# Optimization experiments

Measured on AMD Instinct MI355X. Metric: run time of the kernel, lower is better.

## Reference

```python
import jax, jax.numpy as jnp
import numpy as np

B, P, G, E = 2, 16, 128, 96
C110, C011, C001 = 4, 2, 1
N, CO = 128, 2

def _pw(x, W, b):
    """1x1 conv of any spatial rank == pointwise channel mixing."""
    y = jnp.einsum('oc,bc...->bo...', W, x)
    return y + b.reshape((1, -1) + (1,) * (y.ndim - 2))

def _hidden(s110, s011, s001, Ws, bs):
    # s110:[B,C,P,G,1]  s011:[B,C,1,G,E]  s001:[B,C,1,1,E]
    # sub-stream order: [110 full, 110 pool-P, 110 pool-G, 011 full, 011 pool-G, 011 pool-E, 001]
    t110 = s110[..., 0]         # [B,C,P,G]
    t011 = s011[:, :, 0]        # [B,C,G,E]
    t001 = s001[:, :, 0, 0]     # [B,C,E]
    s = (_pw(t110, Ws[0], bs[0])[..., None]
         + _pw(t110.max(axis=2), Ws[1], bs[1])[:, :, None, :, None]
         + _pw(t110.max(axis=3), Ws[2], bs[2])[:, :, :, None, None]
         + _pw(t011, Ws[3], bs[3])[:, :, None, :, :]
         + _pw(t011.max(axis=2), Ws[4], bs[4])[:, :, None, None, :]
         + _pw(t011.max(axis=3), Ws[5], bs[5])[:, :, None, :, None]
         + _pw(t001, Ws[6], bs[6])[:, :, None, None, :])
    s = jax.nn.leaky_relu(s)    # [B,N,P,G,E]
    return (jnp.max(s, axis=4, keepdims=True),
            jnp.max(s, axis=2, keepdims=True),
            jnp.max(s, axis=(2, 3), keepdims=True))

def _forward(x110, x011, x001, W0_110, b0_110, W0_011, b0_011, W0_001, b0_001, W1, b1, Wact, bact, Wcrit, bcrit):
    Ws0 = [W0_110[0], W0_110[1], W0_110[2], W0_011[0], W0_011[1], W0_011[2], W0_001]
    bs0 = [b0_110[0], b0_110[1], b0_110[2], b0_011[0], b0_011[1], b0_011[2], b0_001]
    s110, s011, s001 = _hidden(x110, x011, x001, Ws0, bs0)
    s110, s011, s001 = _hidden(s110, s011, s001, list(W1), list(b1))
    t110 = s110[..., 0]  # [B,N,P,G]
    # actor head: eliminate G,E via mean pooling (dim_elimination_max_pooling=False)
    a110 = _pw(t110.mean(axis=3), Wact[0], bact[0])              # [B,CO,P]
    a011 = _pw(s011.mean(axis=(3, 4)), Wact[1], bact[1])         # [B,CO,1]
    a001 = _pw(s001[:, :, :, 0].mean(axis=3), Wact[2], bact[2])  # [B,CO,1]
    actions = jax.nn.leaky_relu(a110 + a011 + a001)              # [B,CO,P]
    # critic head: eliminate G via mean pooling
    c110 = _pw(t110.mean(axis=3), Wcrit[0], bcrit[0])            # [B,CO,P]
    c011 = _pw(s011[:, :, 0].mean(axis=2), Wcrit[1], bcrit[1])   # [B,CO,E]
    c001 = _pw(s001[:, :, 0, 0], Wcrit[2], bcrit[2])             # [B,CO,E]
    v = jax.nn.leaky_relu(c110[:, :, :, None] + (c011 + c001)[:, :, None, :])  # [B,CO,P,E]
    v110 = v.max(axis=3).sum(axis=2)  # stream (1,1,0): max over E, sum over P
    v011 = v.max(axis=2).sum(axis=2)  # streams (0,1,1) and (0,0,1) coincide numerically
    values = (2.0 + v110 + 2.0 * v011).reshape(-1)  # python sum(l, 2) starts at 2
    return actions, values

def setup_inputs() -> dict:
    key = jax.random.key(0)
    ks = jax.random.split(key, 12)
    f32 = jnp.float32
    def w(k, shape, fan):
        return jax.random.normal(k, shape, f32) / np.float32(np.sqrt(fan))
    return {
        'x110': jax.random.normal(ks[0], (B, C110, P, G, 1), f32),
        'x011': jax.random.normal(ks[1], (B, C011, 1, G, E), f32),
        'x001': jax.random.normal(ks[2], (B, C001, 1, 1, E), f32),
        'W0_110': w(ks[3], (3, N, C110), C110), 'b0_110': jnp.zeros((3, N), f32),
        'W0_011': w(ks[4], (3, N, C011), C011), 'b0_011': jnp.zeros((3, N), f32),
        'W0_001': w(ks[5], (N, C001), C001),    'b0_001': jnp.zeros((N,), f32),
        'W1':     w(ks[6], (7, N, N), N),       'b1':     jnp.zeros((7, N), f32),
        'Wact':   w(ks[7], (3, CO, N), N),      'bact':   jnp.zeros((3, CO), f32),
        'Wcrit':  w(ks[8], (3, CO, N), N),      'bcrit':  jnp.zeros((3, CO), f32),
    }

def reference(x110, x011, x001, W0_110, b0_110, W0_011, b0_011, W0_001, b0_001, W1, b1, Wact, bact, Wcrit, bcrit):
    return _forward(x110, x011, x001, W0_110, b0_110, W0_011, b0_011, W0_001, b0_001, W1, b1, Wact, bact, Wcrit, bcrit)
```

## Files before the change

kernel.cpp:

```cpp
#include <hip/hip_runtime.h>
#include <math.h>

#define DEVI __device__ __forceinline__

constexpr int B = 2, P = 16, G = 128, E = 96, N = 128, CO = 2;

DEVI float lrelu(float x) { return x > 0.f ? x : 0.01f * x; }

constexpr int OFF_U1     = 0;
constexpr int OFF_V1     = OFF_U1 + 524288;
constexpr int OFF_MAXPU0 = OFF_V1 + 3145728;
constexpr int OFF_MAXEV0 = OFF_MAXPU0 + 32768;
constexpr int OFF_MP110  = OFF_MAXEV0 + 32768;
constexpr int OFF_MG110  = OFF_MP110 + 32768;
constexpr int OFF_S001A  = OFF_MG110 + 4096;
constexpr int OFF_RMP    = OFF_S001A + 24576;
constexpr int OFF_RMG    = OFF_RMP + 1024;
constexpr int OFF_RME    = OFF_RMG + 128;
constexpr int OFF_RMG011 = OFF_RME + 512;
constexpr int OFF_WT     = OFF_RMG011 + 384;
constexpr int OFF_PART   = OFF_WT + 81920;

__global__ void __launch_bounds__(256) k_layer0(
    const float* __restrict__ x110, const float* __restrict__ x011,
    const float* __restrict__ x001,
    const float* __restrict__ W0_110, const float* __restrict__ b0_110,
    const float* __restrict__ W0_011, const float* __restrict__ b0_011,
    const float* __restrict__ W0_001, const float* __restrict__ b0_001,
    const float* __restrict__ W1,
    float* __restrict__ maxpU0g, float* __restrict__ maxeV0g,
    float* __restrict__ mp110, float* __restrict__ mg110,
    float* __restrict__ s001a,
    float* __restrict__ rmpG, float* __restrict__ rmgG,
    float* __restrict__ rmeG, float* __restrict__ rmg011G,
    float* __restrict__ wT) {
  __shared__ float xs[4 * 16 * 128];
  __shared__ float v0h[64 * 97];
  __shared__ float u0[16 * 128];
  __shared__ float rmp[512], rmgS[64], rme[256], rmg011L[192];
  __shared__ float mpu[128], mev[128], part[256];
  const int bn = blockIdx.x, b = bn >> 7, n = bn & 127, tid = threadIdx.x;

  {
    const float4* xsrc = (const float4*)(x110 + (size_t)b * 8192);
    float4* xdst = (float4*)xs;
#pragma unroll
    for (int k = 0; k < 8; k++) xdst[tid + k * 256] = xsrc[tid + k * 256];
  }
  {
    int c = tid >> 7, g = tid & 127;
    const float4* r = (const float4*)(x011 + ((size_t)(b * 2 + c) * 128 + g) * 96);
    float m = -INFINITY;
#pragma unroll
    for (int j = 0; j < 24; j++) {
      float4 v = r[j];
      m = fmaxf(m, fmaxf(fmaxf(v.x, v.y), fmaxf(v.z, v.w)));
    }
    rme[tid] = m;
  }
  __syncthreads();
  for (int i = tid; i < 512; i += 256) {
    int c = i >> 7, g = i & 127;
    float m = -INFINITY;
    for (int p = 0; p < P; p++) m = fmaxf(m, xs[(c * 16 + p) * 128 + g]);
    rmp[i] = m;
  }
  if (tid < 64) {
    int c = tid >> 4, p = tid & 15;
    float m = -INFINITY;
    for (int g = 0; g < G; g++) m = fmaxf(m, xs[(c * 16 + p) * 128 + g]);
    rmgS[tid] = m;
  }
  if (tid < 192) {
    int c = tid / 96, e = tid % 96;
    const float* pp = x011 + ((size_t)(b * 2 + c) * 128) * 96 + e;
    float m = -INFINITY;
    for (int g = 0; g < G; g++) m = fmaxf(m, pp[g * 96]);
    rmg011L[tid] = m;
  }
  __syncthreads();
  float w0[4], w1[4], w2[4];
#pragma unroll
  for (int cc = 0; cc < 4; cc++) {
    w0[cc] = W0_110[n * 4 + cc];
    w1[cc] = W0_110[512 + n * 4 + cc];
    w2[cc] = W0_110[1024 + n * 4 + cc];
  }
  float we0 = W0_011[512 + n * 2], we1 = W0_011[512 + n * 2 + 1];
  float bu = b0_110[n] + b0_110[128 + n] + b0_110[256 + n] + b0_011[256 + n];
  float vw00 = W0_011[n * 2], vw01 = W0_011[n * 2 + 1];
  float vw10 = W0_011[256 + n * 2], vw11 = W0_011[256 + n * 2 + 1];
  float w001 = W0_001[n];
  float bv = b0_011[n] + b0_011[128 + n] + b0_001[n];

#pragma unroll
  for (int k = 0; k < 8; k++) {
    int i = tid + k * 256, p = i >> 7, g = i & 127;
    float acc = bu + we0 * rme[g] + we1 * rme[128 + g];
#pragma unroll
    for (int cc = 0; cc < 4; cc++)
      acc += w0[cc] * xs[(cc * 16 + p) * 128 + g] + w1[cc] * rmp[cc * 128 + g]
           + w2[cc] * rmgS[cc * 16 + p];
    u0[i] = acc;
  }
  __syncthreads();
  if (tid < 128) {
    float m = -INFINITY;
    for (int p = 0; p < P; p++) m = fmaxf(m, u0[p * 128 + tid]);
    mpu[tid] = m;
    maxpU0g[bn * 128 + tid] = m;
  }
  __syncthreads();

  const float* xa = x011 + (size_t)(b * 2) * 12288;
  const float* xb = xa + 12288;
  const float* xc = x001 + b * 96;
  float runMax = -INFINITY;

  for (int h2 = 0; h2 < 2; h2++) {
    for (int k = 0; k < 24; k++) {
      int i = tid + k * 256;
      int gp = i / 96, e = i - gp * 96;
      int g = h2 * 64 + gp;
      float val = bv + vw00 * xa[g * 96 + e] + vw01 * xb[g * 96 + e]
                + vw10 * rmg011L[e] + vw11 * rmg011L[96 + e] + w001 * xc[e];
      v0h[gp * 97 + e] = val;
    }
    __syncthreads();
    {
      int gp = tid & 63, q = tid >> 6;
      const float* r = &v0h[gp * 97 + q * 24];
      float m = -INFINITY;
      for (int j = 0; j < 24; j++) m = fmaxf(m, r[j]);
      part[q * 64 + gp] = m;
    }
    __syncthreads();
    if (tid < 64) {
      float m = fmaxf(fmaxf(part[tid], part[64 + tid]),
                      fmaxf(part[128 + tid], part[192 + tid]));
      int g = h2 * 64 + tid;
      mev[g] = m;
      maxeV0g[bn * 128 + g] = m;
      mp110[bn * 128 + g] = lrelu(mpu[g] + m);
    }
    if (tid < 96) {
      for (int gp = 0; gp < 64; gp++)
        runMax = fmaxf(runMax, mpu[h2 * 64 + gp] + v0h[gp * 97 + tid]);
    }
    __syncthreads();
  }
  {
    int p = tid >> 4, ch = tid & 15;
    float m = -INFINITY;
    for (int g = ch * 8; g < ch * 8 + 8; g++)
      m = fmaxf(m, u0[p * 128 + g] + mev[g]);
    part[tid] = m;
  }
  if (tid < 96) s001a[bn * 96 + tid] = lrelu(runMax);
  __syncthreads();
  if (tid < 16) {
    float m = -INFINITY;
    for (int ch = 0; ch < 16; ch++) m = fmaxf(m, part[tid * 16 + ch]);
    mg110[bn * 16 + tid] = lrelu(m);
  }
  if (n == 0) {
    for (int i = tid; i < 512; i += 256) rmpG[b * 512 + i] = rmp[i];
    if (tid < 64) rmgG[b * 64 + tid] = rmgS[tid];
    rmeG[b * 256 + tid] = rme[tid];
    if (tid < 192) rmg011G[b * 192 + tid] = rmg011L[tid];
  }
  {
    const int gt = bn * 256 + tid;
#pragma unroll
    for (int it = 0; it < 2; it++) {
      int idx = gt + it * 65536;
      if (idx < 81920) {
        int m = idx >> 14, r = idx & 16383;
        int c = r >> 7, nn = r & 127;
        float v;
        if (m == 0)      v = W1[nn * 128 + c];
        else if (m == 1) v = W1[16384 + nn * 128 + c] + W1[5 * 16384 + nn * 128 + c];
        else if (m == 2) v = W1[2 * 16384 + nn * 128 + c];
        else if (m == 3) v = W1[3 * 16384 + nn * 128 + c];
        else             v = W1[4 * 16384 + nn * 128 + c] + W1[6 * 16384 + nn * 128 + c];
        wT[idx] = v;
      }
    }
  }
}

__global__ void __launch_bounds__(512) k_layer1c(
    const float* __restrict__ x110, const float* __restrict__ x011,
    const float* __restrict__ x001,
    const float* __restrict__ W0_110, const float* __restrict__ b0_110,
    const float* __restrict__ W0_011, const float* __restrict__ b0_011,
    const float* __restrict__ W0_001, const float* __restrict__ b0_001,
    const float* __restrict__ maxpU0g, const float* __restrict__ maxeV0g,
    const float* __restrict__ rmpG, const float* __restrict__ rmgG,
    const float* __restrict__ rmeG, const float* __restrict__ rmg011G,
    const float* __restrict__ wT,
    float* __restrict__ U1, float* __restrict__ V1) {
  __shared__ float s110c[128 * 16];
  __shared__ float s011c[128 * 96];
  __shared__ float W0L110[1536], W0L011[768], W0L001[128];
  __shared__ float busum[128], bvsum[128], mpu[128], mev[128];
  __shared__ float x011row[192], rmg011s[192], x001s[96];
  __shared__ float x110col[64], rmg110p[64], rmp4[4], rme2[2];
  const int blk = blockIdx.x;
  const int b = blk >> 7, g = blk & 127;
  const int tid = threadIdx.x;

  for (int i = tid; i < 1536; i += 512) W0L110[i] = W0_110[i];
  for (int i = tid; i < 768; i += 512) W0L011[i] = W0_011[i];
  if (tid < 128) {
    W0L001[tid] = W0_001[tid];
    busum[tid] = b0_110[tid] + b0_110[128 + tid] + b0_110[256 + tid]
               + b0_011[256 + tid];
    bvsum[tid] = b0_011[tid] + b0_011[128 + tid] + b0_001[tid];
    mpu[tid] = maxpU0g[(b * 128 + tid) * 128 + g];
    mev[tid] = maxeV0g[(b * 128 + tid) * 128 + g];
  } else if (tid >= 256 && tid < 448) {
    int i = tid - 256;
    int c = i / 96, e = i % 96;
    x011row[i] = x011[((size_t)(b * 2 + c) * 128 + g) * 96 + e];
    rmg011s[i] = rmg011G[b * 192 + i];
  } else if (tid >= 448 && tid < 512) {
    int i = tid - 448;
    int c = i >> 4, p = i & 15;
    x110col[i] = x110[((size_t)(b * 4 + c) * 16 + p) * 128 + g];
    rmg110p[i] = rmgG[b * 64 + i];
  } else if (tid >= 128 && tid < 224) {
    x001s[tid - 128] = x001[b * 96 + tid - 128];
  } else if (tid >= 224 && tid < 228) {
    rmp4[tid - 224] = rmpG[(b * 4 + tid - 224) * 128 + g];
  } else if (tid >= 228 && tid < 230) {
    rme2[tid - 228] = rmeG[(b * 2 + tid - 228) * 128 + g];
  }
  __syncthreads();

#pragma unroll
  for (int k = 0; k < 4; k++) {
    int i = tid + k * 512, c = i >> 4, p = i & 15;
    float acc = busum[c] + W0L011[512 + c * 2] * rme2[0]
              + W0L011[512 + c * 2 + 1] * rme2[1];
#pragma unroll
    for (int cc = 0; cc < 4; cc++)
      acc += W0L110[c * 4 + cc] * x110col[cc * 16 + p]
           + W0L110[512 + c * 4 + cc] * rmp4[cc]
           + W0L110[1024 + c * 4 + cc] * rmg110p[cc * 16 + p];
    s110c[i] = lrelu(acc + mev[c]);
  }
  for (int k = 0; k < 24; k++) {
    int i = tid + k * 512;
    int c = i / 96, e = i - c * 96;
    float v = bvsum[c]
            + W0L011[c * 2] * x011row[e] + W0L011[c * 2 + 1] * x011row[96 + e]
            + W0L011[256 + c * 2] * rmg011s[e]
            + W0L011[256 + c * 2 + 1] * rmg011s[96 + e]
            + W0L001[c] * x001s[e];
    s011c[i] = lrelu(v + mpu[c]);
  }
  __syncthreads();

  const float* w0T = wT;
  const float* w3T = wT + 3 * 16384;

  if (tid < 256) {
    int n0 = (tid >> 3) * 4, e0 = (tid & 7) * 12;
    float4 acc[4][3];
#pragma unroll
    for (int ni = 0; ni < 4; ni++)
#pragma unroll
      for (int k = 0; k < 3; k++) acc[ni][k] = make_float4(0.f, 0.f, 0.f, 0.f);
    for (int c = 0; c < 128; c++) {
      float4 wv = *(const float4*)&w3T[c * 128 + n0];
      float4 s0 = *(const float4*)&s011c[c * 96 + e0];
      float4 s1 = *(const float4*)&s011c[c * 96 + e0 + 4];
      float4 s2 = *(const float4*)&s011c[c * 96 + e0 + 8];
#pragma unroll
      for (int ni = 0; ni < 4; ni++) {
        float wc = ni == 0 ? wv.x : ni == 1 ? wv.y : ni == 2 ? wv.z : wv.w;
        acc[ni][0].x += wc * s0.x; acc[ni][0].y += wc * s0.y;
        acc[ni][0].z += wc * s0.z; acc[ni][0].w += wc * s0.w;
        acc[ni][1].x += wc * s1.x; acc[ni][1].y += wc * s1.y;
        acc[ni][1].z += wc * s1.z; acc[ni][1].w += wc * s1.w;
        acc[ni][2].x += wc * s2.x; acc[ni][2].y += wc * s2.y;
        acc[ni][2].z += wc * s2.z; acc[ni][2].w += wc * s2.w;
      }
    }
#pragma unroll
    for (int ni = 0; ni < 4; ni++) {
      float* dst = V1 + ((size_t)((b * 128 + g) * 128 + n0 + ni)) * 96 + e0;
#pragma unroll
      for (int k = 0; k < 3; k++) *(float4*)(dst + k * 4) = acc[ni][k];
    }
  } else {
    int t = tid - 256;
    int n = t & 127, ph = t >> 7;
    float a[8];
#pragma unroll
    for (int j = 0; j < 8; j++) a[j] = 0.f;
    for (int c = 0; c < 128; c++) {
      float w0v = w0T[c * 128 + n];
      float4 s0 = *(const float4*)&s110c[c * 16 + ph * 8];
      float4 s1 = *(const float4*)&s110c[c * 16 + ph * 8 + 4];
      a[0] += w0v * s0.x; a[1] += w0v * s0.y; a[2] += w0v * s0.z; a[3] += w0v * s0.w;
      a[4] += w0v * s1.x; a[5] += w0v * s1.y; a[6] += w0v * s1.z; a[7] += w0v * s1.w;
    }
    float* dst = U1 + ((size_t)((b * 128 + g) * 16 + ph * 8)) * 128 + n;
#pragma unroll
    for (int j = 0; j < 8; j++) dst[j * 128] = a[j];
  }
}

__global__ void __launch_bounds__(256) k_post3(
    const float* __restrict__ U1, const float* __restrict__ V1,
    const float* __restrict__ s001a, const float* __restrict__ mp110,
    const float* __restrict__ mg110,
    const float* __restrict__ wT, const float* __restrict__ b1,
    float* __restrict__ partOut) {
  constexpr int GS = 16;
  __shared__ float Vt[GS][8][104];
  __shared__ float Ut[GS][16][9];
  __shared__ float bfL[8][GS];
  __shared__ float egL[8][96];
  __shared__ float cpL[8][16];
  __shared__ float partE[GS][8][4];
  __shared__ float mxeV[GS][8], mxpU[GS][8];
  __shared__ float bbL[8], bvL[8];
  const int blk = blockIdx.x;
  const int b = blk >> 7, nc = (blk >> 3) & 15, gc = blk & 7;
  const int n0 = nc * 8, g0 = gc * 16;
  const int tid = threadIdx.x;
  const float* w15T = wT + 16384;
  const float* w2T  = wT + 2 * 16384;
  const float* w46T = wT + 4 * 16384;

  if (tid < 8) {
    int n = n0 + tid;
    bbL[tid] = b1[n] + b1[128 + n] + b1[256 + n] + b1[640 + n];
    bvL[tid] = b1[384 + n] + b1[512 + n] + b1[768 + n];
  }
  if (tid < 128) {
    int nn = tid >> 4, gl = tid & 15;
    float acc = 0.f;
    for (int c = 0; c < 128; c++)
      acc += w15T[c * 128 + n0 + nn] * mp110[(b * 128 + c) * 128 + g0 + gl];
    bfL[nn][gl] = acc;
  } else {
    int i = tid - 128;
    int nn = i >> 4, p = i & 15;
    float acc = 0.f;
    for (int c = 0; c < 128; c++)
      acc += w2T[c * 128 + n0 + nn] * mg110[(b * 128 + c) * 16 + p];
    cpL[nn][p] = acc;
  }
#pragma unroll
  for (int k = 0; k < 3; k++) {
    int s = tid + k * 256;
    int nn = s / 96, e = s % 96;
    float acc = 0.f;
    for (int c = 0; c < 128; c++)
      acc += w46T[c * 128 + n0 + nn] * s001a[b * 12288 + c * 96 + e];
    egL[nn][e] = acc;
  }
  __syncthreads();

  const size_t Ubase = (size_t)b * 128 * 16 * 128;
  const size_t Vbase = (size_t)b * 128 * 128 * 96;
#pragma unroll
  for (int k = 0; k < 12; k++) {
    int i4 = tid + k * 256;
    int gs = i4 / 192, r = i4 % 192, nn = r / 24, e4 = r % 24;
    float4 v = *(const float4*)(V1 + Vbase
                 + ((size_t)(g0 + gs) * 128 + n0 + nn) * 96 + e4 * 4);
    float bvv = bvL[nn];
    const float* eg = &egL[nn][e4 * 4];
    float4 o = make_float4(v.x + bvv + eg[0], v.y + bvv + eg[1],
                           v.z + bvv + eg[2], v.w + bvv + eg[3]);
    *(float4*)&Vt[gs][nn][e4 * 4] = o;
  }
#pragma unroll
  for (int k = 0; k < 8; k++) {
    int i = tid + k * 256;
    int gs = i >> 7, r = i & 127, p = r >> 3, nn = r & 7;
    float u = U1[Ubase + ((size_t)(g0 + gs) * 16 + p) * 128 + n0 + nn];
    Ut[gs][p][nn] = u + bbL[nn] + cpL[nn][p] + bfL[nn][gs];
  }
  __syncthreads();
#pragma unroll
  for (int k = 0; k < 2; k++) {
    int i = tid + k * 256;
    int gs = i >> 5, nn = (i >> 2) & 7, ec = i & 3;
    float m = -INFINITY;
    for (int e = ec * 24; e < ec * 24 + 24; e++) m = fmaxf(m, Vt[gs][nn][e]);
    partE[gs][nn][ec] = m;
  }
  __syncthreads();
  if (tid < 128) {
    int gs = tid >> 3, nn = tid & 7;
    mxeV[gs][nn] = fmaxf(fmaxf(partE[gs][nn][0], partE[gs][nn][1]),
                         fmaxf(partE[gs][nn][2], partE[gs][nn][3]));
    float m = -INFINITY;
    for (int p = 0; p < 16; p++) m = fmaxf(m, Ut[gs][p][nn]);
    mxpU[gs][nn] = m;
  }
  __syncthreads();

  float* pb = partOut + (size_t)blk * 1664;
  if (tid < 128) {
    int nn = tid >> 4, p = tid & 15;
    float a = 0.f;
#pragma unroll
    for (int gs = 0; gs < GS; gs++)
      a += lrelu(Ut[gs][p][nn] + mxeV[gs][nn]);
    pb[tid] = a;
  }
#pragma unroll
  for (int k = 0; k < 3; k++) {
    int s = tid + k * 256;
    int nn = s / 96, e = s % 96;
    float a = 0.f, m = -INFINITY;
#pragma unroll
    for (int gs = 0; gs < GS; gs++) {
      float pre = mxpU[gs][nn] + Vt[gs][nn][e];
      a += lrelu(pre);
      m = fmaxf(m, pre);
    }
    pb[128 + s] = a;
    pb[896 + s] = m;
  }
}

__global__ void __launch_bounds__(256) k_final(
    const float* __restrict__ partIn,
    const float* __restrict__ Wact, const float* __restrict__ bact,
    const float* __restrict__ Wcrit, const float* __restrict__ bcrit,
    float* __restrict__ out) {
  __shared__ float buf[128][97];
  __shared__ float m110s[128][17];
  __shared__ float sm011[N], sm001[N], sce1[E], sce[E], scp[P], srow[P], scol[E];
  const int bo = blockIdx.x;
  const int o = bo & 1, b = bo >> 1;
  const int t = threadIdx.x;
  const float* pbB = partIn + (size_t)(b * 16) * 8 * 1664;

#pragma unroll
  for (int k = 0; k < 8; k++) {
    int i = t + k * 256;
    int nc = i >> 7, j = i & 127;
    const float* base = pbB + (size_t)(nc * 8) * 1664;
    float a = 0.f;
#pragma unroll
    for (int gc = 0; gc < 8; gc++) a += base[gc * 1664 + j];
    m110s[nc * 8 + (j >> 4)][j & 15] = a * (1.f / G);
  }
#pragma unroll
  for (int k = 0; k < 48; k++) {
    int i = t + k * 256;
    int nc = i / 768, r = i % 768;
    const float* base = pbB + (size_t)(nc * 8) * 1664;
    float a = 0.f;
#pragma unroll
    for (int gc = 0; gc < 8; gc++) a += base[gc * 1664 + 128 + r];
    buf[nc * 8 + r / 96][r % 96] = a * (1.f / G);
  }
  __syncthreads();
  if (t < 128) {
    float s = 0.f;
    for (int e = 0; e < E; e++) s += buf[t][e];
    sm011[t] = s * (1.f / E);
  }
  if (t < 96) {
    const float* wc1 = Wcrit + (1 * CO + o) * N;
    float c = 0.f;
    for (int n = 0; n < N; n++) c += wc1[n] * buf[n][t];
    sce1[t] = c;
  }
  __syncthreads();
#pragma unroll
  for (int k = 0; k < 48; k++) {
    int i = t + k * 256;
    int nc = i / 768, r = i % 768;
    const float* base = pbB + (size_t)(nc * 8) * 1664;
    float m = -INFINITY;
#pragma unroll
    for (int gc = 0; gc < 8; gc++) m = fmaxf(m, base[gc * 1664 + 896 + r]);
    buf[nc * 8 + r / 96][r % 96] = lrelu(m);
  }
  __syncthreads();
  if (t < 128) {
    float s = 0.f;
    for (int e = 0; e < E; e++) s += buf[t][e];
    sm001[t] = s * (1.f / E);
  }
  if (t < 96) {
    const float* wc2 = Wcrit + (2 * CO + o) * N;
    float c = 0.f;
    for (int n = 0; n < N; n++) c += wc2[n] * buf[n][t];
    sce[t] = sce1[t] + c + bcrit[CO + o] + bcrit[2 * CO + o];
  }
  __syncthreads();
  if (t < P) {
    const float* wa0 = Wact + o * N;
    const float* wa1 = Wact + (1 * CO + o) * N;
    const float* wa2 = Wact + (2 * CO + o) * N;
    const float* wc0 = Wcrit + o * N;
    float a = 0.f, c = 0.f, aa = 0.f;
    for (int n = 0; n < N; n++) {
      float m = m110s[n][t];
      a += wa0[n] * m;
      c += wc0[n] * m;
      aa += wa1[n] * sm011[n] + wa2[n] * sm001[n];
    }
    float act = a + aa + bact[o] + bact[CO + o] + bact[2 * CO + o];
    out[(b * CO + o) * P + t] = lrelu(act);
    scp[t] = c + bcrit[o];
  }
  __syncthreads();
  if (t < P) {
    float m = -INFINITY;
    for (int e = 0; e < E; e++) m = fmaxf(m, lrelu(scp[t] + sce[e]));
    srow[t] = m;
  } else if (t < P + E) {
    int e = t - P;
    float m = -INFINITY;
    for (int p = 0; p < P; p++) m = fmaxf(m, lrelu(scp[p] + sce[e]));
    scol[e] = m;
  }
  __syncthreads();
  if (t == 0) {
    float v110 = 0.f, v011 = 0.f;
    for (int p = 0; p < P; p++) v110 += srow[p];
    for (int e = 0; e < E; e++) v011 += scol[e];
    out[B * CO * P + b * CO + o] = 2.f + v110 + 2.f * v011;
  }
}

extern "C" void kernel_launch(void* const* d_in, const int* in_sizes, int n_in,
                              void* d_out, int out_size, void* d_ws, size_t ws_size,
                              hipStream_t stream) {
  const float* x110   = (const float*)d_in[0];
  const float* x011   = (const float*)d_in[1];
  const float* x001   = (const float*)d_in[2];
  const float* W0_110 = (const float*)d_in[3];
  const float* b0_110 = (const float*)d_in[4];
  const float* W0_011 = (const float*)d_in[5];
  const float* b0_011 = (const float*)d_in[6];
  const float* W0_001 = (const float*)d_in[7];
  const float* b0_001 = (const float*)d_in[8];
  const float* W1     = (const float*)d_in[9];
  const float* b1     = (const float*)d_in[10];
  const float* Wact   = (const float*)d_in[11];
  const float* bact   = (const float*)d_in[12];
  const float* Wcrit  = (const float*)d_in[13];
  const float* bcrit  = (const float*)d_in[14];
  float* out = (float*)d_out;
  float* w = (float*)d_ws;

  float* U1     = w + OFF_U1;
  float* V1     = w + OFF_V1;
  float* maxpU0 = w + OFF_MAXPU0;
  float* maxeV0 = w + OFF_MAXEV0;
  float* mp110  = w + OFF_MP110;
  float* mg110  = w + OFF_MG110;
  float* s001a  = w + OFF_S001A;
  float* rmpG   = w + OFF_RMP;
  float* rmgG   = w + OFF_RMG;
  float* rmeG   = w + OFF_RME;
  float* rmg011 = w + OFF_RMG011;
  float* wT     = w + OFF_WT;
  float* partB  = w + OFF_PART;

  k_layer0<<<256, 256, 0, stream>>>(x110, x011, x001, W0_110, b0_110, W0_011,
                                    b0_011, W0_001, b0_001, W1,
                                    maxpU0, maxeV0, mp110, mg110, s001a,
                                    rmpG, rmgG, rmeG, rmg011, wT);
  k_layer1c<<<256, 512, 0, stream>>>(x110, x011, x001, W0_110, b0_110, W0_011,
                                     b0_011, W0_001, b0_001,
                                     maxpU0, maxeV0, rmpG, rmgG, rmeG, rmg011,
                                     wT, U1, V1);
  k_post3<<<256, 256, 0, stream>>>(U1, V1, s001a, mp110, mg110, wT, b1, partB);
  k_final<<<4, 256, 0, stream>>>(partB, Wact, bact, Wcrit, bcrit, out);
}
```

Baseline: 119.9 us.

## Split layer kernels across G/N halves and move input reductions to a prep kernel

Measured after the change: 133.3 us. 1.11x slower.

```diff
diff --git a/kernel.cpp b/kernel.cpp
--- a/kernel.cpp
+++ b/kernel.cpp
@@ -9,17 +9,67 @@
 
 constexpr int OFF_U1     = 0;
 constexpr int OFF_V1     = OFF_U1 + 524288;
-constexpr int OFF_MAXPU0 = OFF_V1 + 3145728;
-constexpr int OFF_MAXEV0 = OFF_MAXPU0 + 32768;
-constexpr int OFF_MP110  = OFF_MAXEV0 + 32768;
-constexpr int OFF_MG110  = OFF_MP110 + 32768;
-constexpr int OFF_S001A  = OFF_MG110 + 4096;
-constexpr int OFF_RMP    = OFF_S001A + 24576;
+constexpr int OFF_MP110  = OFF_V1 + 3145728;
+constexpr int OFF_MGP    = OFF_MP110 + 32768;
+constexpr int OFF_S1P    = OFF_MGP + 8192;
+constexpr int OFF_RMP    = OFF_S1P + 49152;
 constexpr int OFF_RMG    = OFF_RMP + 1024;
 constexpr int OFF_RME    = OFF_RMG + 128;
 constexpr int OFF_RMG011 = OFF_RME + 512;
 constexpr int OFF_WT     = OFF_RMG011 + 384;
 constexpr int OFF_PART   = OFF_WT + 81920;
+
+__global__ void __launch_bounds__(256) k_prep(
+    const float* __restrict__ x110, const float* __restrict__ x011,
+    const float* __restrict__ W1,
+    float* __restrict__ rmpG, float* __restrict__ rmgG,
+    float* __restrict__ rmeG, float* __restrict__ rmg011G,
+    float* __restrict__ wT) {
+  const int blk = blockIdx.x, tid = threadIdx.x;
+  if (blk < 56) {
+    for (int idx = blk * 256 + tid; idx < 81920; idx += 56 * 256) {
+      int m = idx >> 14, r = idx & 16383;
+      int c = r >> 7, nn = r & 127;
+      float v;
+      if (m == 0)      v = W1[nn * 128 + c];
+      else if (m == 1) v = W1[16384 + nn * 128 + c] + W1[5 * 16384 + nn * 128 + c];
+      else if (m == 2) v = W1[2 * 16384 + nn * 128 + c];
+      else if (m == 3) v = W1[3 * 16384 + nn * 128 + c];
+      else             v = W1[4 * 16384 + nn * 128 + c] + W1[6 * 16384 + nn * 128 + c];
+      wT[idx] = v;
+    }
+  } else {
+    int t = (blk - 56) * 256 + tid;
+    if (t < 1024) {
+      int g = t & 127, c = (t >> 7) & 3, b = t >> 9;
+      const float* base = x110 + ((b * 4 + c) * P) * G + g;
+      float m = -INFINITY;
+      for (int p = 0; p < P; p++) m = fmaxf(m, base[p * G]);
+      rmpG[t] = m;
+    } else if (t < 1152) {
+      int i = t - 1024;
+      int p = i & 15, c = (i >> 4) & 3, b = i >> 6;
+      const float* base = x110 + ((b * 4 + c) * P + p) * G;
+      float m = -INFINITY;
+      for (int g = 0; g < G; g++) m = fmaxf(m, base[g]);
+      rmgG[i] = m;
+    } else if (t < 1664) {
+      int i = t - 1152;
+      int g = i & 127, c = (i >> 7) & 1, b = i >> 8;
+      const float* base = x011 + ((size_t)(b * 2 + c) * G + g) * E;
+      float m = -INFINITY;
+      for (int e = 0; e < E; e++) m = fmaxf(m, base[e]);
+      rmeG[i] = m;
+    } else if (t < 2048) {
+      int i = t - 1664;
+      int e = i % 96; int r = i / 96; int c = r & 1, b = r >> 1;
+      const float* base = x011 + ((size_t)(b * 2 + c) * G) * E + e;
+      float m = -INFINITY;
+      for (int g = 0; g < G; g++) m = fmaxf(m, base[g * E]);
+      rmg011G[i] = m;
+    }
+  }
+}
 
 __global__ void __launch_bounds__(256) k_layer0(
     const float* __restrict__ x110, const float* __restrict__ x011,
@@ -27,58 +77,40 @@
     const float* __restrict__ W0_110, const float* __restrict__ b0_110,
     const float* __restrict__ W0_011, const float* __restrict__ b0_011,
     const float* __restrict__ W0_001, const float* __restrict__ b0_001,
-    const float* __restrict__ W1,
-    float* __restrict__ maxpU0g, float* __restrict__ maxeV0g,
-    float* __restrict__ mp110, float* __restrict__ mg110,
-    float* __restrict__ s001a,
-    float* __restrict__ rmpG, float* __restrict__ rmgG,
-    float* __restrict__ rmeG, float* __restrict__ rmg011G,
-    float* __restrict__ wT) {
-  __shared__ float xs[4 * 16 * 128];
+    const float* __restrict__ rmpG, const float* __restrict__ rmgG,
+    const float* __restrict__ rmeG, const float* __restrict__ rmg011G,
+    float* __restrict__ mp110, float* __restrict__ mgp,
+    float* __restrict__ s1p) {
+  __shared__ float xs[4 * 16 * 64];
   __shared__ float v0h[64 * 97];
-  __shared__ float u0[16 * 128];
-  __shared__ float rmp[512], rmgS[64], rme[256], rmg011L[192];
-  __shared__ float mpu[128], mev[128], part[256];
-  const int bn = blockIdx.x, b = bn >> 7, n = bn & 127, tid = threadIdx.x;
-
-  {
-    const float4* xsrc = (const float4*)(x110 + (size_t)b * 8192);
-    float4* xdst = (float4*)xs;
-#pragma unroll
-    for (int k = 0; k < 8; k++) xdst[tid + k * 256] = xsrc[tid + k * 256];
-  }
-  {
-    int c = tid >> 7, g = tid & 127;
-    const float4* r = (const float4*)(x011 + ((size_t)(b * 2 + c) * 128 + g) * 96);
-    float m = -INFINITY;
-#pragma unroll
-    for (int j = 0; j < 24; j++) {
-      float4 v = r[j];
-      m = fmaxf(m, fmaxf(fmaxf(v.x, v.y), fmaxf(v.z, v.w)));
-    }
-    rme[tid] = m;
-  }
-  __syncthreads();
-  for (int i = tid; i < 512; i += 256) {
-    int c = i >> 7, g = i & 127;
-    float m = -INFINITY;
-    for (int p = 0; p < P; p++) m = fmaxf(m, xs[(c * 16 + p) * 128 + g]);
-    rmp[i] = m;
-  }
-  if (tid < 64) {
-    int c = tid >> 4, p = tid & 15;
-    float m = -INFINITY;
-    for (int g = 0; g < G; g++) m = fmaxf(m, xs[(c * 16 + p) * 128 + g]);
-    rmgS[tid] = m;
-  }
-  if (tid < 192) {
-    int c = tid / 96, e = tid % 96;
-    const float* pp = x011 + ((size_t)(b * 2 + c) * 128) * 96 + e;
-    float m = -INFINITY;
-    for (int g = 0; g < G; g++) m = fmaxf(m, pp[g * 96]);
-    rmg011L[tid] = m;
-  }
-  __syncthreads();
+  __shared__ float u0h[16 * 64];
+  __shared__ float rmpL[256], rmeL[128], rmgSL[64], rmg011L[192], x001L[96];
+  __shared__ float mpu[64], mev[64], part[256];
+  const int blk = blockIdx.x;
+  const int b = blk >> 8, n = (blk >> 1) & 127, gh = blk & 1;
+  const int bn = b * 128 + n, g0 = gh * 64;
+  const int tid = threadIdx.x;
+
+#pragma unroll
+  for (int k = 0; k < 4; k++) {
+    int i4 = tid + k * 256;
+    int g4 = i4 & 15, p = (i4 >> 4) & 15, cc = i4 >> 8;
+    *(float4*)&xs[(cc * 16 + p) * 64 + g4 * 4] =
+        *(const float4*)(x110 + ((size_t)(b * 4 + cc) * 16 + p) * 128 + g0 + g4 * 4);
+  }
+  if (tid < 256) {
+    int cc = tid >> 6, gp = tid & 63;
+    rmpL[tid] = rmpG[b * 512 + cc * 128 + g0 + gp];
+  }
+  if (tid < 128) {
+    int c2 = tid >> 6, gp = tid & 63;
+    rmeL[tid] = rmeG[b * 256 + c2 * 128 + g0 + gp];
+  }
+  if (tid < 64) rmgSL[tid] = rmgG[b * 64 + tid];
+  if (tid < 192) rmg011L[tid] = rmg011G[b * 192 + tid];
+  if (tid < 96) x001L[tid] = x001[b * 96 + tid];
+  __syncthreads();
+
   float w0[4], w1[4], w2[4];
 #pragma unroll
   for (int cc = 0; cc < 4; cc++) {
@@ -94,108 +126,76 @@
   float bv = b0_011[n] + b0_011[128 + n] + b0_001[n];
 
 #pragma unroll
-  for (int k = 0; k < 8; k++) {
-    int i = tid + k * 256, p = i >> 7, g = i & 127;
-    float acc = bu + we0 * rme[g] + we1 * rme[128 + g];
+  for (int k = 0; k < 4; k++) {
+    int i = tid + k * 256, p = i >> 6, gp = i & 63;
+    float acc = bu + we0 * rmeL[gp] + we1 * rmeL[64 + gp];
 #pragma unroll
     for (int cc = 0; cc < 4; cc++)
-      acc += w0[cc] * xs[(cc * 16 + p) * 128 + g] + w1[cc] * rmp[cc * 128 + g]
-           + w2[cc] * rmgS[cc * 16 + p];
-    u0[i] = acc;
-  }
-  __syncthreads();
-  if (tid < 128) {
-    float m = -INFINITY;
-    for (int p = 0; p < P; p++) m = fmaxf(m, u0[p * 128 + tid]);
-    mpu[tid] = m;
-    maxpU0g[bn * 128 + tid] = m;
-  }
-  __syncthreads();
-
-  const float* xa = x011 + (size_t)(b * 2) * 12288;
-  const float* xb = xa + 12288;
-  const float* xc = x001 + b * 96;
-  float runMax = -INFINITY;
-
-  for (int h2 = 0; h2 < 2; h2++) {
+      acc += w0[cc] * xs[(cc * 16 + p) * 64 + gp] + w1[cc] * rmpL[cc * 64 + gp]
+           + w2[cc] * rmgSL[cc * 16 + p];
+    u0h[i] = acc;
+  }
+  {
+    const float* xa = x011 + (size_t)(b * 2) * 12288;
+    const float* xb = xa + 12288;
+#pragma unroll
     for (int k = 0; k < 24; k++) {
       int i = tid + k * 256;
       int gp = i / 96, e = i - gp * 96;
-      int g = h2 * 64 + gp;
+      int g = g0 + gp;
       float val = bv + vw00 * xa[g * 96 + e] + vw01 * xb[g * 96 + e]
-                + vw10 * rmg011L[e] + vw11 * rmg011L[96 + e] + w001 * xc[e];
+                + vw10 * rmg011L[e] + vw11 * rmg011L[96 + e] + w001 * x001L[e];
       v0h[gp * 97 + e] = val;
     }
-    __syncthreads();
-    {
-      int gp = tid & 63, q = tid >> 6;
-      const float* r = &v0h[gp * 97 + q * 24];
-      float m = -INFINITY;
-      for (int j = 0; j < 24; j++) m = fmaxf(m, r[j]);
-      part[q * 64 + gp] = m;
-    }
-    __syncthreads();
-    if (tid < 64) {
-      float m = fmaxf(fmaxf(part[tid], part[64 + tid]),
-                      fmaxf(part[128 + tid], part[192 + tid]));
-      int g = h2 * 64 + tid;
-      mev[g] = m;
-      maxeV0g[bn * 128 + g] = m;
-      mp110[bn * 128 + g] = lrelu(mpu[g] + m);
-    }
-    if (tid < 96) {
-      for (int gp = 0; gp < 64; gp++)
-        runMax = fmaxf(runMax, mpu[h2 * 64 + gp] + v0h[gp * 97 + tid]);
-    }
-    __syncthreads();
-  }
+  }
+  __syncthreads();
+  {
+    int gp = tid & 63, q = tid >> 6;
+    const float* r = &v0h[gp * 97 + q * 24];
+    float m = -INFINITY;
+    for (int j = 0; j < 24; j++) m = fmaxf(m, r[j]);
+    part[q * 64 + gp] = m;
+  }
+  if (tid < 64) {
+    float m = -INFINITY;
+    for (int p = 0; p < P; p++) m = fmaxf(m, u0h[p * 64 + tid]);
+    mpu[tid] = m;
+  }
+  __syncthreads();
+  if (tid < 64) {
+    float m = fmaxf(fmaxf(part[tid], part[64 + tid]),
+                    fmaxf(part[128 + tid], part[192 + tid]));
+    mev[tid] = m;
+    mp110[bn * 128 + g0 + tid] = lrelu(mpu[tid] + m);
+  }
+  __syncthreads();
   {
     int p = tid >> 4, ch = tid & 15;
     float m = -INFINITY;
-    for (int g = ch * 8; g < ch * 8 + 8; g++)
-      m = fmaxf(m, u0[p * 128 + g] + mev[g]);
+    for (int gp = ch * 4; gp < ch * 4 + 4; gp++)
+      m = fmaxf(m, u0h[p * 64 + gp] + mev[gp]);
     part[tid] = m;
   }
-  if (tid < 96) s001a[bn * 96 + tid] = lrelu(runMax);
   __syncthreads();
   if (tid < 16) {
     float m = -INFINITY;
     for (int ch = 0; ch < 16; ch++) m = fmaxf(m, part[tid * 16 + ch]);
-    mg110[bn * 16 + tid] = lrelu(m);
-  }
-  if (n == 0) {
-    for (int i = tid; i < 512; i += 256) rmpG[b * 512 + i] = rmp[i];
-    if (tid < 64) rmgG[b * 64 + tid] = rmgS[tid];
-    rmeG[b * 256 + tid] = rme[tid];
-    if (tid < 192) rmg011G[b * 192 + tid] = rmg011L[tid];
-  }
-  {
-    const int gt = bn * 256 + tid;
-#pragma unroll
-    for (int it = 0; it < 2; it++) {
-      int idx = gt + it * 65536;
-      if (idx < 81920) {
-        int m = idx >> 14, r = idx & 16383;
-        int c = r >> 7, nn = r & 127;
-        float v;
-        if (m == 0)      v = W1[nn * 128 + c];
-        else if (m == 1) v = W1[16384 + nn * 128 + c] + W1[5 * 16384 + nn * 128 + c];
-        else if (m == 2) v = W1[2 * 16384 + nn * 128 + c];
-        else if (m == 3) v = W1[3 * 16384 + nn * 128 + c];
-        else             v = W1[4 * 16384 + nn * 128 + c] + W1[6 * 16384 + nn * 128 + c];
-        wT[idx] = v;
-      }
-    }
+    mgp[(bn * 2 + gh) * 16 + tid] = m;
+  }
+  if (tid < 96) {
+    float m = -INFINITY;
+    for (int gp = 0; gp < 64; gp++)
+      m = fmaxf(m, mpu[gp] + v0h[gp * 97 + tid]);
+    s1p[(bn * 2 + gh) * 96 + tid] = m;
   }
 }
 
-__global__ void __launch_bounds__(512) k_layer1c(
+__global__ void __launch_bounds__(256) k_layer1(
     const float* __restrict__ x110, const float* __restrict__ x011,
     const float* __restrict__ x001,
     const float* __restrict__ W0_110, const float* __restrict__ b0_110,
     const float* __restrict__ W0_011, const float* __restrict__ b0_011,
     const float* __restrict__ W0_001, const float* __restrict__ b0_001,
-    const float* __restrict__ maxpU0g, const float* __restrict__ maxeV0g,
     const float* __restrict__ rmpG, const float* __restrict__ rmgG,
     const float* __restrict__ rmeG, const float* __restrict__ rmg011G,
     const float* __restrict__ wT,
@@ -206,41 +206,38 @@
   __shared__ float busum[128], bvsum[128], mpu[128], mev[128];
   __shared__ float x011row[192], rmg011s[192], x001s[96];
   __shared__ float x110col[64], rmg110p[64], rmp4[4], rme2[2];
+  __shared__ float partM[256];
   const int blk = blockIdx.x;
-  const int b = blk >> 7, g = blk & 127;
+  const int b = blk >> 8, g = (blk >> 1) & 127, nh = blk & 1;
+  const int n0 = nh * 64;
   const int tid = threadIdx.x;
 
-  for (int i = tid; i < 1536; i += 512) W0L110[i] = W0_110[i];
-  for (int i = tid; i < 768; i += 512) W0L011[i] = W0_011[i];
+  for (int i = tid; i < 1536; i += 256) W0L110[i] = W0_110[i];
+  for (int i = tid; i < 768; i += 256) W0L011[i] = W0_011[i];
   if (tid < 128) {
     W0L001[tid] = W0_001[tid];
     busum[tid] = b0_110[tid] + b0_110[128 + tid] + b0_110[256 + tid]
                + b0_011[256 + tid];
     bvsum[tid] = b0_011[tid] + b0_011[128 + tid] + b0_001[tid];
-    mpu[tid] = maxpU0g[(b * 128 + tid) * 128 + g];
-    mev[tid] = maxeV0g[(b * 128 + tid) * 128 + g];
-  } else if (tid >= 256 && tid < 448) {
-    int i = tid - 256;
-    int c = i / 96, e = i % 96;
-    x011row[i] = x011[((size_t)(b * 2 + c) * 128 + g) * 96 + e];
-    rmg011s[i] = rmg011G[b * 192 + i];
-  } else if (tid >= 448 && tid < 512) {
-    int i = tid - 448;
-    int c = i >> 4, p = i & 15;
-    x110col[i] = x110[((size_t)(b * 4 + c) * 16 + p) * 128 + g];
-    rmg110p[i] = rmgG[b * 64 + i];
-  } else if (tid >= 128 && tid < 224) {
-    x001s[tid - 128] = x001[b * 96 + tid - 128];
-  } else if (tid >= 224 && tid < 228) {
-    rmp4[tid - 224] = rmpG[(b * 4 + tid - 224) * 128 + g];
-  } else if (tid >= 228 && tid < 230) {
-    rme2[tid - 228] = rmeG[(b * 2 + tid - 228) * 128 + g];
-  }
-  __syncthreads();
-
-#pragma unroll
-  for (int k = 0; k < 4; k++) {
-    int i = tid + k * 512, c = i >> 4, p = i & 15;
+  }
+  if (tid < 192) {
+    int c = tid / 96, e = tid % 96;
+    x011row[tid] = x011[((size_t)(b * 2 + c) * 128 + g) * 96 + e];
+    rmg011s[tid] = rmg011G[b * 192 + tid];
+  }
+  if (tid < 96) x001s[tid] = x001[b * 96 + tid];
+  if (tid < 64) {
+    int c = tid >> 4, p = tid & 15;
+    x110col[tid] = x110[((size_t)(b * 4 + c) * 16 + p) * 128 + g];
+    rmg110p[tid] = rmgG[b * 64 + tid];
+  }
+  if (tid < 4) rmp4[tid] = rmpG[(b * 4 + tid) * 128 + g];
+  if (tid < 2) rme2[tid] = rmeG[(b * 2 + tid) * 128 + g];
+  __syncthreads();
+
+#pragma unroll
+  for (int k = 0; k < 8; k++) {
+    int i = tid + k * 256, c = i >> 4, p = i & 15;
     float acc = busum[c] + W0L011[512 + c * 2] * rme2[0]
               + W0L011[512 + c * 2 + 1] * rme2[1];
 #pragma unroll
@@ -248,75 +245,101 @@
       acc += W0L110[c * 4 + cc] * x110col[cc * 16 + p]
            + W0L110[512 + c * 4 + cc] * rmp4[cc]
            + W0L110[1024 + c * 4 + cc] * rmg110p[cc * 16 + p];
-    s110c[i] = lrelu(acc + mev[c]);
-  }
-  for (int k = 0; k < 24; k++) {
-    int i = tid + k * 512;
+    s110c[i] = acc;
+  }
+  for (int k = 0; k < 48; k++) {
+    int i = tid + k * 256;
     int c = i / 96, e = i - c * 96;
     float v = bvsum[c]
             + W0L011[c * 2] * x011row[e] + W0L011[c * 2 + 1] * x011row[96 + e]
             + W0L011[256 + c * 2] * rmg011s[e]
             + W0L011[256 + c * 2 + 1] * rmg011s[96 + e]
             + W0L001[c] * x001s[e];
-    s011c[i] = lrelu(v + mpu[c]);
+    s011c[i] = v;
+  }
+  __syncthreads();
+  if (tid < 128) {
+    float m = -INFINITY;
+    for (int p = 0; p < P; p++) m = fmaxf(m, s110c[tid * 16 + p]);
+    mpu[tid] = m;
+  }
+  {
+    int c = tid >> 1, h = tid & 1;
+    const float* r = &s011c[c * 96 + h * 48];
+    float m = -INFINITY;
+    for (int j = 0; j < 48; j++) m = fmaxf(m, r[j]);
+    partM[tid] = m;
+  }
+  __syncthreads();
+  if (tid < 128) mev[tid] = fmaxf(partM[tid * 2], partM[tid * 2 + 1]);
+  __syncthreads();
+#pragma unroll
+  for (int k = 0; k < 8; k++) {
+    int i = tid + k * 256, c = i >> 4;
+    s110c[i] = lrelu(s110c[i] + mev[c]);
+  }
+  for (int k = 0; k < 48; k++) {
+    int i = tid + k * 256, c = i / 96;
+    s011c[i] = lrelu(s011c[i] + mpu[c]);
   }
   __syncthreads();
 
   const float* w0T = wT;
   const float* w3T = wT + 3 * 16384;
 
-  if (tid < 256) {
-    int n0 = (tid >> 3) * 4, e0 = (tid & 7) * 12;
-    float4 acc[4][3];
-#pragma unroll
-    for (int ni = 0; ni < 4; ni++)
-#pragma unroll
-      for (int k = 0; k < 3; k++) acc[ni][k] = make_float4(0.f, 0.f, 0.f, 0.f);
+  {
+    int np = tid >> 3, e0 = (tid & 7) * 12;
+    int na = n0 + np * 2, nb = na + 1;
+    float4 aA[3], aB[3];
+#pragma unroll
+    for (int k = 0; k < 3; k++) {
+      aA[k] = make_float4(0.f, 0.f, 0.f, 0.f);
+      aB[k] = make_float4(0.f, 0.f, 0.f, 0.f);
+    }
     for (int c = 0; c < 128; c++) {
-      float4 wv = *(const float4*)&w3T[c * 128 + n0];
+      float2 wv = *(const float2*)&w3T[c * 128 + na];
       float4 s0 = *(const float4*)&s011c[c * 96 + e0];
       float4 s1 = *(const float4*)&s011c[c * 96 + e0 + 4];
       float4 s2 = *(const float4*)&s011c[c * 96 + e0 + 8];
-#pragma unroll
-      for (int ni = 0; ni < 4; ni++) {
-        float wc = ni == 0 ? wv.x : ni == 1 ? wv.y : ni == 2 ? wv.z : wv.w;
-        acc[ni][0].x += wc * s0.x; acc[ni][0].y += wc * s0.y;
-        acc[ni][0].z += wc * s0.z; acc[ni][0].w += wc * s0.w;
-        acc[ni][1].x += wc * s1.x; acc[ni][1].y += wc * s1.y;
-        acc[ni][1].z += wc * s1.z; acc[ni][1].w += wc * s1.w;
-        acc[ni][2].x += wc * s2.x; acc[ni][2].y += wc * s2.y;
-        acc[ni][2].z += wc * s2.z; acc[ni][2].w += wc * s2.w;
-      }
-    }
-#pragma unroll
-    for (int ni = 0; ni < 4; ni++) {
-      float* dst = V1 + ((size_t)((b * 128 + g) * 128 + n0 + ni)) * 96 + e0;
-#pragma unroll
-      for (int k = 0; k < 3; k++) *(float4*)(dst + k * 4) = acc[ni][k];
-    }
-  } else {
-    int t = tid - 256;
-    int n = t & 127, ph = t >> 7;
-    float a[8];
-#pragma unroll
-    for (int j = 0; j < 8; j++) a[j] = 0.f;
+      aA[0].x += wv.x * s0.x; aA[0].y += wv.x * s0.y;
+      aA[0].z += wv.x * s0.z; aA[0].w += wv.x * s0.w;
+      aA[1].x += wv.x * s1.x; aA[1].y += wv.x * s1.y;
+      aA[1].z += wv.x * s1.z; aA[1].w += wv.x * s1.w;
+      aA[2].x += wv.x * s2.x; aA[2].y += wv.x * s2.y;
+      aA[2].z += wv.x * s2.z; aA[2].w += wv.x * s2.w;
+      aB[0].x += wv.y * s0.x; aB[0].y += wv.y * s0.y;
+      aB[0].z += wv.y * s0.z; aB[0].w += wv.y * s0.w;
+      aB[1].x += wv.y * s1.x; aB[1].y += wv.y * s1.y;
+      aB[1].z += wv.y * s1.z; aB[1].w += wv.y * s1.w;
+      aB[2].x += wv.y * s2.x; aB[2].y += wv.y * s2.y;
+      aB[2].z += wv.y * s2.z; aB[2].w += wv.y * s2.w;
+    }
+    float* dA = V1 + ((size_t)((b * 128 + g) * 128 + na)) * 96 + e0;
+    float* dB = dA + 96;
+#pragma unroll
+    for (int k = 0; k < 3; k++) {
+      *(float4*)(dA + k * 4) = aA[k];
+      *(float4*)(dB + k * 4) = aB[k];
+    }
+  }
+  {
+    int nn = tid >> 2, pq = tid & 3;
+    int n = n0 + nn;
+    float4 a = make_float4(0.f, 0.f, 0.f, 0.f);
+    const float* sr = &s110c[pq * 4];
     for (int c = 0; c < 128; c++) {
       float w0v = w0T[c * 128 + n];
-      float4 s0 = *(const float4*)&s110c[c * 16 + ph * 8];
-      float4 s1 = *(const float4*)&s110c[c * 16 + ph * 8 + 4];
-      a[0] += w0v * s0.x; a[1] += w0v * s0.y; a[2] += w0v * s0.z; a[3] += w0v * s0.w;
-      a[4] += w0v * s1.x; a[5] += w0v * s1.y; a[6] += w0v * s1.z; a[7] += w0v * s1.w;
-    }
-    float* dst = U1 + ((size_t)((b * 128 + g) * 16 + ph * 8)) * 128 + n;
-#pragma unroll
-    for (int j = 0; j < 8; j++) dst[j * 128] = a[j];
+      float4 s = *(const float4*)&sr[c * 16];
+      a.x += w0v * s.x; a.y += w0v * s.y; a.z += w0v * s.z; a.w += w0v * s.w;
+    }
+    *(float4*)(U1 + ((size_t)((b * 128 + g) * 128 + n)) * 16 + pq * 4) = a;
   }
 }
 
 __global__ void __launch_bounds__(256) k_post3(
     const float* __restrict__ U1, const float* __restrict__ V1,
-    const float* __restrict__ s001a, const float* __restrict__ mp110,
-    const float* __restrict__ mg110,
+    const float* __restrict__ s1p, const float* __restrict__ mp110,
+    const float* __restrict__ mgp,
     const float* __restrict__ wT, const float* __restrict__ b1,
     float* __restrict__ partOut) {
   constexpr int GS = 16;
@@ -351,8 +374,10 @@
     int i = tid - 128;
     int nn = i >> 4, p = i & 15;
     float acc = 0.f;
-    for (int c = 0; c < 128; c++)
-      acc += w2T[c * 128 + n0 + nn] * mg110[(b * 128 + c) * 16 + p];
+    for (int c = 0; c < 128; c++) {
+      float m = fmaxf(mgp[(b * 128 + c) * 32 + p], mgp[(b * 128 + c) * 32 + 16 + p]);
+      acc += w2T[c * 128 + n0 + nn] * lrelu(m);
+    }
     cpL[nn][p] = acc;
   }
 #pragma unroll
@@ -360,13 +385,15 @@
     int s = tid + k * 256;
     int nn = s / 96, e = s % 96;
     float acc = 0.f;
-    for (int c = 0; c < 128; c++)
-      acc += w46T[c * 128 + n0 + nn] * s001a[b * 12288 + c * 96 + e];
+    for (int c = 0; c < 128; c++) {
+      float m = fmaxf(s1p[(b * 128 + c) * 192 + e], s1p[(b * 128 + c) * 192 + 96 + e]);
+      acc += w46T[c * 128 + n0 + nn] * lrelu(m);
+    }
     egL[nn][e] = acc;
   }
   __syncthreads();
 
-  const size_t Ubase = (size_t)b * 128 * 16 * 128;
+  const size_t Ubase = (size_t)b * 128 * 128 * 16;
   const size_t Vbase = (size_t)b * 128 * 128 * 96;
 #pragma unroll
   for (int k = 0; k < 12; k++) {
@@ -381,11 +408,16 @@
     *(float4*)&Vt[gs][nn][e4 * 4] = o;
   }
 #pragma unroll
-  for (int k = 0; k < 8; k++) {
-    int i = tid + k * 256;
-    int gs = i >> 7, r = i & 127, p = r >> 3, nn = r & 7;
-    float u = U1[Ubase + ((size_t)(g0 + gs) * 16 + p) * 128 + n0 + nn];
-    Ut[gs][p][nn] = u + bbL[nn] + cpL[nn][p] + bfL[nn][gs];
+  for (int k = 0; k < 2; k++) {
+    int i4 = tid + k * 256;
+    int gs = i4 >> 5, r = i4 & 31, nn = r >> 2, p4 = r & 3;
+    float4 u = *(const float4*)(U1 + Ubase
+                 + ((size_t)(g0 + gs) * 128 + n0 + nn) * 16 + p4 * 4);
+    float base = bbL[nn] + bfL[nn][gs];
+    Ut[gs][p4 * 4 + 0][nn] = u.x + base + cpL[nn][p4 * 4 + 0];
+    Ut[gs][p4 * 4 + 1][nn] = u.y + base + cpL[nn][p4 * 4 + 1];
+    Ut[gs][p4 * 4 + 2][nn] = u.z + base + cpL[nn][p4 * 4 + 2];
+    Ut[gs][p4 * 4 + 3][nn] = u.w + base + cpL[nn][p4 * 4 + 3];
   }
   __syncthreads();
 #pragma unroll
@@ -560,11 +592,9 @@
 
   float* U1     = w + OFF_U1;
   float* V1     = w + OFF_V1;
-  float* maxpU0 = w + OFF_MAXPU0;
-  float* maxeV0 = w + OFF_MAXEV0;
   float* mp110  = w + OFF_MP110;
-  float* mg110  = w + OFF_MG110;
-  float* s001a  = w + OFF_S001A;
+  float* mgp    = w + OFF_MGP;
+  float* s1p    = w + OFF_S1P;
   float* rmpG   = w + OFF_RMP;
   float* rmgG   = w + OFF_RMG;
   float* rmeG   = w + OFF_RME;
@@ -572,14 +602,14 @@
   float* wT     = w + OFF_WT;
   float* partB  = w + OFF_PART;
 
-  k_layer0<<<256, 256, 0, stream>>>(x110, x011, x001, W0_110, b0_110, W0_011,
-                                    b0_011, W0_001, b0_001, W1,
-                                    maxpU0, maxeV0, mp110, mg110, s001a,
-                                    rmpG, rmgG, rmeG, rmg011, wT);
-  k_layer1c<<<256, 512, 0, stream>>>(x110, x011, x001, W0_110, b0_110, W0_011,
-                                     b0_011, W0_001, b0_001,
-                                     maxpU0, maxeV0, rmpG, rmgG, rmeG, rmg011,
-                                     wT, U1, V1);
-  k_post3<<<256, 256, 0, stream>>>(U1, V1, s001a, mp110, mg110, wT, b1, partB);
+  k_prep<<<64, 256, 0, stream>>>(x110, x011, W1, rmpG, rmgG, rmeG, rmg011, wT);
+  k_layer0<<<512, 256, 0, stream>>>(x110, x011, x001, W0_110, b0_110, W0_011,
+                                    b0_011, W0_001, b0_001,
+                                    rmpG, rmgG, rmeG, rmg011,
+                                    mp110, mgp, s1p);
+  k_layer1<<<512, 256, 0, stream>>>(x110, x011, x001, W0_110, b0_110, W0_011,
+                                    b0_011, W0_001, b0_001,
+                                    rmpG, rmgG, rmeG, rmg011, wT, U1, V1);
+  k_post3<<<256, 256, 0, stream>>>(U1, V1, s1p, mp110, mgp, wT, b1, partB);
   k_final<<<4, 256, 0, stream>>>(partB, Wact, bact, Wcrit, bcrit, out);
 }
```
